# Kernel tuning notes

Measured on AMD Instinct MI355X. Metric: run time of the kernel, lower is better.

Reference implementation:

```python
import jax, jax.numpy as jnp
import numpy as np

B, S, H, D, P = 16, 512, 12, 768, 256
TOP_RATE = 0.1
K = int(round(TOP_RATE * S))  # 51, matches round(self.top_rate * hidden_state.size(1))
LN_EPS = 1e-5


def setup_inputs() -> dict:
    key = jax.random.key(0)
    ks = jax.random.split(key, 6)
    return {
        "hidden_state": jax.random.normal(ks[0], (B, S, D), dtype=jnp.float32),
        "attention": jax.random.normal(ks[1], (B, H, S, S), dtype=jnp.float32),
        "length": S,  # uniform valid length (scalar int)
        # node_trans: Linear(D, P)
        "W_node": jax.random.normal(ks[2], (D, P), dtype=jnp.float32) * 0.02,
        "b_node": jnp.zeros((P,), dtype=jnp.float32),
        # node_eta parameter, initialized to 0 (self.node_eta.data.fill_(0))
        "node_eta": jnp.zeros((1,), dtype=jnp.float32),
        # fc: Linear(P, P)
        "W_fc": jax.random.normal(ks[3], (P, P), dtype=jnp.float32) * 0.02,
        "b_fc": jnp.zeros((P,), dtype=jnp.float32),
        # LayerNorm(P)
        "ln_gamma": jnp.ones((P,), dtype=jnp.float32),
        "ln_beta": jnp.zeros((P,), dtype=jnp.float32),
    }


def reference(hidden_state, attention, W_node, b_node, node_eta, W_fc, b_fc,
              ln_gamma, ln_beta, length):
    # average attention over heads: [B, S, S]
    avg_atten = attention.mean(axis=1)
    # per-target-node top-k neighbors
    vals, idx = jax.lax.top_k(avg_atten, K)  # [B, S, K]
    # edge mask replicating softmax(where(v>0, v, -1e9)) followed by nonzero():
    # entries at -1e9 underflow to exactly 0 in fp32 softmax iff the row has a
    # positive value; otherwise the softmax is uniform and all edges survive.
    keep = vals > 0.0
    row_has_pos = keep.any(axis=-1, keepdims=True)
    keep = jnp.where(row_has_pos, keep, True)            # [B, S, K] (>=1 True per row)
    keepf = keep.astype(hidden_state.dtype)[..., None]   # [B, S, K, 1]

    # node_trans on all nodes: [B, S, P]
    h = hidden_state @ W_node + b_node

    # gather source-node features h[b, idx[b, t, j], :] -> [B, S, K, P]
    gathered = jax.vmap(lambda hb, ib: hb[ib])(h, idx)

    # reduce='mean': edge weight w=1, mailbox mean over kept incoming edges
    h_agg = (gathered * keepf).sum(axis=2) / keepf.sum(axis=2)

    eta = node_eta[0]
    new_h = eta * h + (1.0 - eta) * h_agg                # [B, S, P]

    # dgl.mean_nodes: mean over the `length` nodes of each sub-graph (=S here)
    out = new_h.mean(axis=1)                             # [B, P]

    # fc(dropout(tanh(out))) with dropout in eval mode (identity)
    out = jnp.tanh(out) @ W_fc + b_fc

    # LayerNorm
    mu = out.mean(axis=-1, keepdims=True)
    var = ((out - mu) ** 2).mean(axis=-1, keepdims=True)
    out = (out - mu) / jnp.sqrt(var + LN_EPS) * ln_gamma + ln_beta
    return out
```

## Files before the change

kernel.cpp:

```cpp
#include <hip/hip_runtime.h>
#include <math.h>

#define B_ 16
#define S_ 512
#define H_ 12
#define D_ 768
#define P_ 256
#define K_ 51
#define CH_ 16
#define NCHUNK_ (S_/CH_)

#define WAVE_SYNC() asm volatile("s_waitcnt lgkmcnt(0)" ::: "memory")

__device__ __forceinline__ unsigned okey(float f) {
  unsigned u = __float_as_uint(f);
  return (u & 0x80000000u) ? ~u : (u | 0x80000000u);
}

__global__ __launch_bounds__(256) void k1_topk_weights(
    const float* __restrict__ attn, float* __restrict__ w) {
  const int tid = threadIdx.x;
  const int wv = tid >> 6;
  const int lane = tid & 63;
  const int bt = blockIdx.x * 4 + wv;
  const int b = bt >> 9;
  const int t = bt & (S_ - 1);

  __shared__ __align__(16) unsigned hist[4][256];

  *(uint4*)&hist[wv][4 * lane] = uint4{0u, 0u, 0u, 0u};

  const float* base = attn + (((size_t)b * H_) * S_ + t) * S_;
  float a[8] = {0.f, 0.f, 0.f, 0.f, 0.f, 0.f, 0.f, 0.f};
  #pragma unroll
  for (int h = 0; h < H_; ++h) {
    const float* r = base + (size_t)h * (S_ * S_);
    const float4 u = *(const float4*)(r + 4 * lane);
    const float4 v = *(const float4*)(r + 256 + 4 * lane);
    a[0] += u.x; a[1] += u.y; a[2] += u.z; a[3] += u.w;
    a[4] += v.x; a[5] += v.y; a[6] += v.z; a[7] += v.w;
  }
  unsigned k[8];
  #pragma unroll
  for (int i = 0; i < 8; ++i) {
    a[i] *= (1.0f / (float)H_);
    k[i] = okey(a[i]);
  }

  int p = 0;
  #pragma unroll
  for (int i = 0; i < 8; ++i) p += __popcll(__ballot(a[i] > 0.f));

  bool sel[8];
  float invcnt;
  if (p >= 1 && p < K_) {
    #pragma unroll
    for (int i = 0; i < 8; ++i) sel[i] = (a[i] > 0.f);
    invcnt = 1.0f / (float)p;
  } else {
    unsigned prefix = 0;
    int remaining = K_;
    int tieCnt = 0;
    bool exited = false;
    unsigned exitm = 0;
    for (int pass = 0; pass < 4; ++pass) {
      const int shift = 24 - 8 * pass;
      const unsigned pm = (pass == 0) ? 0u : (0xFFFFFFFFu << (shift + 8));
      WAVE_SYNC();
      #pragma unroll
      for (int i = 0; i < 8; ++i)
        if ((k[i] & pm) == prefix)
          atomicAdd(&hist[wv][(k[i] >> shift) & 255u], 1u);
      WAVE_SYNC();
      const uint4 c4 = *(uint4*)&hist[wv][4 * lane];
      *(uint4*)&hist[wv][4 * lane] = uint4{0u, 0u, 0u, 0u};
      const unsigned loc = c4.x + c4.y + c4.z + c4.w;
      unsigned suf = loc;
      #pragma unroll
      for (int off = 1; off < 64; off <<= 1) {
        const unsigned vv = __shfl_down(suf, off, 64);
        if (lane + off < 64) suf += vv;
      }
      const unsigned after = suf - loc;
      const unsigned s3 = after + c4.w;
      const unsigned s2 = s3 + c4.z;
      const unsigned s1 = s2 + c4.y;
      const unsigned s0 = s1 + c4.x;
      const unsigned rem = (unsigned)remaining;
      int dig = 0, abv = 0, tie = 0;
      bool found = false;
      if (s0 >= rem && s1 < rem)         { dig = 4*lane+0; abv = (int)s1;    tie = (int)(s0 - s1);    found = true; }
      else if (s1 >= rem && s2 < rem)    { dig = 4*lane+1; abv = (int)s2;    tie = (int)(s1 - s2);    found = true; }
      else if (s2 >= rem && s3 < rem)    { dig = 4*lane+2; abv = (int)s3;    tie = (int)(s2 - s3);    found = true; }
      else if (s3 >= rem && after < rem) { dig = 4*lane+3; abv = (int)after; tie = (int)(s3 - after); found = true; }
      const unsigned long long fm = __ballot(found);
      const int src = __ffsll((unsigned long long)fm) - 1;
      dig = __shfl(dig, src, 64);
      abv = __shfl(abv, src, 64);
      tie = __shfl(tie, src, 64);
      prefix |= ((unsigned)dig) << shift;
      remaining -= abv;
      tieCnt = tie;
      if (tieCnt == remaining) {
        exited = true;
        exitm = (shift == 0) ? 0xFFFFFFFFu : (0xFFFFFFFFu << shift);
        break;
      }
    }
    if (exited) {
      #pragma unroll
      for (int i = 0; i < 8; ++i) sel[i] = (k[i] & exitm) >= prefix;
    } else {
      const unsigned T = prefix;
      unsigned long long m[8];
      #pragma unroll
      for (int i = 0; i < 8; ++i) m[i] = __ballot(k[i] == T);
      const unsigned long long lt = ((unsigned long long)1 << lane) - 1ull;
      int fh = 0;
      #pragma unroll
      for (int i = 0; i < 4; ++i) fh += __popcll(m[i]);
      #pragma unroll
      for (int i = 0; i < 8; ++i) {
        sel[i] = (k[i] > T);
        if (k[i] == T) {
          int r = 0;
          if (i < 4) {
            #pragma unroll
            for (int i2 = 0; i2 < 4; ++i2) r += __popcll(m[i2] & lt);
            for (int i2 = 0; i2 < i; ++i2) r += (int)((m[i2] >> lane) & 1ull);
          } else {
            r = fh;
            #pragma unroll
            for (int i2 = 4; i2 < 8; ++i2) r += __popcll(m[i2] & lt);
            for (int i2 = 4; i2 < i; ++i2) r += (int)((m[i2] >> lane) & 1ull);
          }
          if (r < remaining) sel[i] = true;
        }
      }
    }
    invcnt = 1.0f / (float)K_;
  }

  float* wrow = w + b * S_;
  #pragma unroll
  for (int i = 0; i < 8; ++i) {
    const int col = (i < 4) ? (4 * lane + i) : (256 + 4 * lane + (i - 4));
    if (sel[i]) atomicAdd(&wrow[col], invcnt);
  }
}

__global__ __launch_bounds__(192) void k2_weighted_sum(
    const float* __restrict__ hidden, const float* __restrict__ w,
    const float* __restrict__ node_eta, float* __restrict__ x) {
  const int chunk = blockIdx.x;
  const int b = blockIdx.y;
  const int tid = threadIdx.x;
  __shared__ float coef[CH_];
  if (tid < CH_) {
    const float eta = node_eta[0];
    const float wv = w[b * S_ + chunk * CH_ + tid];
    coef[tid] = (eta + (1.0f - eta) * wv) * (1.0f / (float)S_);
  }
  __syncthreads();
  const float* hb = hidden + ((size_t)b * S_ + (size_t)chunk * CH_) * D_ + 4 * tid;
  float4 acc = make_float4(0.f, 0.f, 0.f, 0.f);
  #pragma unroll
  for (int s = 0; s < CH_; ++s) {
    const float4 v = *(const float4*)(hb + (size_t)s * D_);
    const float c = coef[s];
    acc.x += c * v.x; acc.y += c * v.y; acc.z += c * v.z; acc.w += c * v.w;
  }
  float* xp = x + b * D_ + 4 * tid;
  atomicAdd(xp + 0, acc.x);
  atomicAdd(xp + 1, acc.y);
  atomicAdd(xp + 2, acc.z);
  atomicAdd(xp + 3, acc.w);
}

__global__ __launch_bounds__(256) void k3a_tanh_matvec(
    const float* __restrict__ x, const float* __restrict__ W_node,
    const float* __restrict__ b_node, float* __restrict__ tbuf) {
  const int j = blockIdx.x;
  const int b = blockIdx.y;
  const int tid = threadIdx.x;
  const int pp = tid & 15;
  const int g = tid >> 4;
  __shared__ float xs[D_];
  __shared__ float part[16][32];
  for (int d = tid; d < D_; d += 256) xs[d] = x[b * D_ + d];
  __syncthreads();
  const float* Wp = W_node + 32 * j + 2 * pp;
  float2 acc = make_float2(0.f, 0.f);
  const int d0 = 48 * g;
  #pragma unroll 8
  for (int dd = 0; dd < 48; ++dd) {
    const int d = d0 + dd;
    const float2 wv = *(const float2*)(Wp + (size_t)d * P_);
    const float xv = xs[d];
    acc.x += xv * wv.x; acc.y += xv * wv.y;
  }
  *(float2*)&part[g][2 * pp] = acc;
  __syncthreads();
  if (tid < 32) {
    float s = 0.f;
    #pragma unroll
    for (int gg = 0; gg < 16; ++gg) s += part[gg][tid];
    const int pcol = 32 * j + tid;
    tbuf[b * P_ + pcol] = tanhf(s + b_node[pcol]);
  }
}

__global__ __launch_bounds__(256) void k3b_fc(
    const float* __restrict__ tbuf, const float* __restrict__ W_fc,
    const float* __restrict__ b_fc, float* __restrict__ obuf) {
  const int j = blockIdx.x;
  const int b = blockIdx.y;
  const int tid = threadIdx.x;
  const int pp = tid & 31;
  const int g = tid >> 5;
  __shared__ float ts[P_];
  __shared__ float part[8][64];
  ts[tid] = tbuf[b * P_ + tid];
  __syncthreads();
  const float* Wp = W_fc + 64 * j + 2 * pp;
  float2 acc = make_float2(0.f, 0.f);
  const int q0 = 32 * g;
  #pragma unroll 8
  for (int qq = 0; qq < 32; ++qq) {
    const int q = q0 + qq;
    const float2 wv = *(const float2*)(Wp + (size_t)q * P_);
    const float tv = ts[q];
    acc.x += tv * wv.x; acc.y += tv * wv.y;
  }
  *(float2*)&part[g][2 * pp] = acc;
  __syncthreads();
  if (tid < 64) {
    float s = 0.f;
    #pragma unroll
    for (int gg = 0; gg < 8; ++gg) s += part[gg][tid];
    const int pcol = 64 * j + tid;
    obuf[b * P_ + pcol] = s + b_fc[pcol];
  }
}

__global__ __launch_bounds__(256) void k3c_layernorm(
    const float* __restrict__ obuf, const float* __restrict__ gamma,
    const float* __restrict__ beta, float* __restrict__ out) {
  const int b = blockIdx.x;
  const int tid = threadIdx.x;
  __shared__ float red[4];
  const float o = obuf[b * P_ + tid];
  float s = o;
  #pragma unroll
  for (int off = 32; off > 0; off >>= 1) s += __shfl_down(s, off, 64);
  const int wave = tid >> 6, lane = tid & 63;
  if (lane == 0) red[wave] = s;
  __syncthreads();
  const float mu = (red[0] + red[1] + red[2] + red[3]) * (1.0f / (float)P_);
  __syncthreads();
  const float dv = o - mu;
  float s2 = dv * dv;
  #pragma unroll
  for (int off = 32; off > 0; off >>= 1) s2 += __shfl_down(s2, off, 64);
  if (lane == 0) red[wave] = s2;
  __syncthreads();
  const float var = (red[0] + red[1] + red[2] + red[3]) * (1.0f / (float)P_);
  const float inv = 1.0f / sqrtf(var + 1e-5f);
  out[b * P_ + tid] = dv * inv * gamma[tid] + beta[tid];
}

extern "C" void kernel_launch(void* const* d_in, const int* in_sizes, int n_in,
                              void* d_out, int out_size, void* d_ws, size_t ws_size,
                              hipStream_t stream) {
  (void)in_sizes; (void)n_in; (void)out_size; (void)ws_size;
  const float* hidden   = (const float*)d_in[0];
  const float* attn     = (const float*)d_in[1];
  const float* W_node   = (const float*)d_in[3];
  const float* b_node   = (const float*)d_in[4];
  const float* node_eta = (const float*)d_in[5];
  const float* W_fc     = (const float*)d_in[6];
  const float* b_fc     = (const float*)d_in[7];
  const float* gamma    = (const float*)d_in[8];
  const float* beta     = (const float*)d_in[9];
  float* out = (float*)d_out;

  float* w    = (float*)d_ws;
  float* x    = w + B_ * S_;
  float* tbuf = x + B_ * D_;
  float* obuf = tbuf + B_ * P_;
  hipMemsetAsync(d_ws, 0, (size_t)(B_ * S_ + B_ * D_) * sizeof(float), stream);

  k1_topk_weights<<<(B_ * S_) / 4, 256, 0, stream>>>(attn, w);
  k2_weighted_sum<<<dim3(NCHUNK_, B_), 192, 0, stream>>>(hidden, w, node_eta, x);
  k3a_tanh_matvec<<<dim3(8, B_), 256, 0, stream>>>(x, W_node, b_node, tbuf);
  k3b_fc<<<dim3(4, B_), 256, 0, stream>>>(tbuf, W_fc, b_fc, obuf);
  k3c_layernorm<<<B_, 256, 0, stream>>>(obuf, gamma, beta, out);
}
```

Measured before the change: 340.7 us.

## Replace float atomics with bitmask ballots, bitwise radix select, fuse fc+layernorm

The top-k kernel now writes per-row selection bitmasks and an inverse count instead of doing global float atomicAdds into the column weight array. A new kernel sums those masks per column into the final coefficients. The radix select switches from an LDS histogram with atomics to a 32-pass bitwise select using ballot counts. The fc and layernorm kernels are merged into one launch, which removes one launch and the weight memset but adds a column-sum kernel that has low parallelism.

```diff
diff --git a/kernel.cpp b/kernel.cpp
--- a/kernel.cpp
+++ b/kernel.cpp
@@ -10,25 +10,20 @@
 #define CH_ 16
 #define NCHUNK_ (S_/CH_)
 
-#define WAVE_SYNC() asm volatile("s_waitcnt lgkmcnt(0)" ::: "memory")
-
 __device__ __forceinline__ unsigned okey(float f) {
   unsigned u = __float_as_uint(f);
   return (u & 0x80000000u) ? ~u : (u | 0x80000000u);
 }
 
-__global__ __launch_bounds__(256) void k1_topk_weights(
-    const float* __restrict__ attn, float* __restrict__ w) {
+__global__ __launch_bounds__(256) void k1_topk_mask(
+    const float* __restrict__ attn, unsigned long long* __restrict__ maskbuf,
+    float* __restrict__ invbuf) {
   const int tid = threadIdx.x;
   const int wv = tid >> 6;
   const int lane = tid & 63;
   const int bt = blockIdx.x * 4 + wv;
   const int b = bt >> 9;
   const int t = bt & (S_ - 1);
-
-  __shared__ __align__(16) unsigned hist[4][256];
-
-  *(uint4*)&hist[wv][4 * lane] = uint4{0u, 0u, 0u, 0u};
 
   const float* base = attn + (((size_t)b * H_) * S_ + t) * S_;
   float a[8] = {0.f, 0.f, 0.f, 0.f, 0.f, 0.f, 0.f, 0.f};
@@ -59,66 +54,33 @@
     invcnt = 1.0f / (float)p;
   } else {
     unsigned prefix = 0;
-    int remaining = K_;
-    int tieCnt = 0;
-    bool exited = false;
-    unsigned exitm = 0;
-    for (int pass = 0; pass < 4; ++pass) {
-      const int shift = 24 - 8 * pass;
-      const unsigned pm = (pass == 0) ? 0u : (0xFFFFFFFFu << (shift + 8));
-      WAVE_SYNC();
+    int rem = K_;
+    bool done = false;
+    unsigned dmask = 0, thr = 0;
+    for (int bpos = 31; bpos >= 0; --bpos) {
+      const unsigned bit = 1u << bpos;
+      const unsigned mb = ~(bit - 1u);
+      const unsigned cand = prefix | bit;
+      int cnt = 0;
       #pragma unroll
       for (int i = 0; i < 8; ++i)
-        if ((k[i] & pm) == prefix)
-          atomicAdd(&hist[wv][(k[i] >> shift) & 255u], 1u);
-      WAVE_SYNC();
-      const uint4 c4 = *(uint4*)&hist[wv][4 * lane];
-      *(uint4*)&hist[wv][4 * lane] = uint4{0u, 0u, 0u, 0u};
-      const unsigned loc = c4.x + c4.y + c4.z + c4.w;
-      unsigned suf = loc;
-      #pragma unroll
-      for (int off = 1; off < 64; off <<= 1) {
-        const unsigned vv = __shfl_down(suf, off, 64);
-        if (lane + off < 64) suf += vv;
-      }
-      const unsigned after = suf - loc;
-      const unsigned s3 = after + c4.w;
-      const unsigned s2 = s3 + c4.z;
-      const unsigned s1 = s2 + c4.y;
-      const unsigned s0 = s1 + c4.x;
-      const unsigned rem = (unsigned)remaining;
-      int dig = 0, abv = 0, tie = 0;
-      bool found = false;
-      if (s0 >= rem && s1 < rem)         { dig = 4*lane+0; abv = (int)s1;    tie = (int)(s0 - s1);    found = true; }
-      else if (s1 >= rem && s2 < rem)    { dig = 4*lane+1; abv = (int)s2;    tie = (int)(s1 - s2);    found = true; }
-      else if (s2 >= rem && s3 < rem)    { dig = 4*lane+2; abv = (int)s3;    tie = (int)(s2 - s3);    found = true; }
-      else if (s3 >= rem && after < rem) { dig = 4*lane+3; abv = (int)after; tie = (int)(s3 - after); found = true; }
-      const unsigned long long fm = __ballot(found);
-      const int src = __ffsll((unsigned long long)fm) - 1;
-      dig = __shfl(dig, src, 64);
-      abv = __shfl(abv, src, 64);
-      tie = __shfl(tie, src, 64);
-      prefix |= ((unsigned)dig) << shift;
-      remaining -= abv;
-      tieCnt = tie;
-      if (tieCnt == remaining) {
-        exited = true;
-        exitm = (shift == 0) ? 0xFFFFFFFFu : (0xFFFFFFFFu << shift);
-        break;
-      }
+        cnt += __popcll(__ballot((k[i] & mb) == cand));
+      if (cnt == rem) { done = true; dmask = mb; thr = cand; break; }
+      if (cnt > rem) prefix = cand;
+      else rem -= cnt;
     }
-    if (exited) {
-      #pragma unroll
-      for (int i = 0; i < 8; ++i) sel[i] = (k[i] & exitm) >= prefix;
+    if (done) {
+      #pragma unroll
+      for (int i = 0; i < 8; ++i) sel[i] = (k[i] & dmask) >= thr;
     } else {
       const unsigned T = prefix;
-      unsigned long long m[8];
-      #pragma unroll
-      for (int i = 0; i < 8; ++i) m[i] = __ballot(k[i] == T);
+      unsigned long long mm[8];
+      #pragma unroll
+      for (int i = 0; i < 8; ++i) mm[i] = __ballot(k[i] == T);
       const unsigned long long lt = ((unsigned long long)1 << lane) - 1ull;
       int fh = 0;
       #pragma unroll
-      for (int i = 0; i < 4; ++i) fh += __popcll(m[i]);
+      for (int i = 0; i < 4; ++i) fh += __popcll(mm[i]);
       #pragma unroll
       for (int i = 0; i < 8; ++i) {
         sel[i] = (k[i] > T);
@@ -126,48 +88,79 @@
           int r = 0;
           if (i < 4) {
             #pragma unroll
-            for (int i2 = 0; i2 < 4; ++i2) r += __popcll(m[i2] & lt);
-            for (int i2 = 0; i2 < i; ++i2) r += (int)((m[i2] >> lane) & 1ull);
+            for (int i2 = 0; i2 < 4; ++i2) r += __popcll(mm[i2] & lt);
+            for (int i2 = 0; i2 < i; ++i2) r += (int)((mm[i2] >> lane) & 1ull);
           } else {
             r = fh;
             #pragma unroll
-            for (int i2 = 4; i2 < 8; ++i2) r += __popcll(m[i2] & lt);
-            for (int i2 = 4; i2 < i; ++i2) r += (int)((m[i2] >> lane) & 1ull);
+            for (int i2 = 4; i2 < 8; ++i2) r += __popcll(mm[i2] & lt);
+            for (int i2 = 4; i2 < i; ++i2) r += (int)((mm[i2] >> lane) & 1ull);
           }
-          if (r < remaining) sel[i] = true;
+          if (r < rem) sel[i] = true;
         }
       }
     }
     invcnt = 1.0f / (float)K_;
   }
 
-  float* wrow = w + b * S_;
-  #pragma unroll
-  for (int i = 0; i < 8; ++i) {
-    const int col = (i < 4) ? (4 * lane + i) : (256 + 4 * lane + (i - 4));
-    if (sel[i]) atomicAdd(&wrow[col], invcnt);
-  }
+  unsigned long long m[8];
+  #pragma unroll
+  for (int i = 0; i < 8; ++i) m[i] = __ballot(sel[i]);
+  if (lane == 0) {
+    ulonglong2* mp = (ulonglong2*)(maskbuf + (size_t)bt * 8);
+    mp[0] = ulonglong2{m[0], m[1]};
+    mp[1] = ulonglong2{m[2], m[3]};
+    mp[2] = ulonglong2{m[4], m[5]};
+    mp[3] = ulonglong2{m[6], m[7]};
+    invbuf[bt] = invcnt;
+  }
+}
+
+__global__ __launch_bounds__(256) void k1b_colsum(
+    const unsigned long long* __restrict__ maskbuf,
+    const float* __restrict__ invbuf, const float* __restrict__ node_eta,
+    float* __restrict__ coef) {
+  const int half = blockIdx.x;
+  const int b = blockIdx.y;
+  const int tid = threadIdx.x;
+  __shared__ unsigned long long ms[S_][8];
+  __shared__ float inv[S_];
+
+  const ulonglong2* mrow2 = (const ulonglong2*)(maskbuf + (size_t)b * S_ * 8);
+  ulonglong2* lds2 = (ulonglong2*)&ms[0][0];
+  #pragma unroll
+  for (int j = 0; j < 8; ++j) lds2[tid + 256 * j] = mrow2[tid + 256 * j];
+  inv[tid] = invbuf[b * S_ + tid];
+  inv[tid + 256] = invbuf[b * S_ + tid + 256];
+  __syncthreads();
+
+  const int s = half * 256 + tid;
+  const int wi = (s < 256) ? (s & 3) : 4 + (s & 3);
+  const unsigned long long bitm = 1ull << ((s & 255) >> 2);
+  float w = 0.f;
+  #pragma unroll 8
+  for (int tt = 0; tt < S_; ++tt)
+    if (ms[tt][wi] & bitm) w += inv[tt];
+
+  const float eta = node_eta[0];
+  coef[b * S_ + s] = (eta + (1.0f - eta) * w) * (1.0f / (float)S_);
 }
 
 __global__ __launch_bounds__(192) void k2_weighted_sum(
-    const float* __restrict__ hidden, const float* __restrict__ w,
-    const float* __restrict__ node_eta, float* __restrict__ x) {
+    const float* __restrict__ hidden, const float* __restrict__ coef,
+    float* __restrict__ x) {
   const int chunk = blockIdx.x;
   const int b = blockIdx.y;
   const int tid = threadIdx.x;
-  __shared__ float coef[CH_];
-  if (tid < CH_) {
-    const float eta = node_eta[0];
-    const float wv = w[b * S_ + chunk * CH_ + tid];
-    coef[tid] = (eta + (1.0f - eta) * wv) * (1.0f / (float)S_);
-  }
+  __shared__ float cs[CH_];
+  if (tid < CH_) cs[tid] = coef[b * S_ + chunk * CH_ + tid];
   __syncthreads();
   const float* hb = hidden + ((size_t)b * S_ + (size_t)chunk * CH_) * D_ + 4 * tid;
   float4 acc = make_float4(0.f, 0.f, 0.f, 0.f);
   #pragma unroll
   for (int s = 0; s < CH_; ++s) {
     const float4 v = *(const float4*)(hb + (size_t)s * D_);
-    const float c = coef[s];
+    const float c = cs[s];
     acc.x += c * v.x; acc.y += c * v.y; acc.z += c * v.z; acc.w += c * v.w;
   }
   float* xp = x + b * D_ + 4 * tid;
@@ -210,46 +203,21 @@
   }
 }
 
-__global__ __launch_bounds__(256) void k3b_fc(
+__global__ __launch_bounds__(256) void k3bc_fc_ln(
     const float* __restrict__ tbuf, const float* __restrict__ W_fc,
-    const float* __restrict__ b_fc, float* __restrict__ obuf) {
-  const int j = blockIdx.x;
-  const int b = blockIdx.y;
-  const int tid = threadIdx.x;
-  const int pp = tid & 31;
-  const int g = tid >> 5;
-  __shared__ float ts[P_];
-  __shared__ float part[8][64];
-  ts[tid] = tbuf[b * P_ + tid];
-  __syncthreads();
-  const float* Wp = W_fc + 64 * j + 2 * pp;
-  float2 acc = make_float2(0.f, 0.f);
-  const int q0 = 32 * g;
-  #pragma unroll 8
-  for (int qq = 0; qq < 32; ++qq) {
-    const int q = q0 + qq;
-    const float2 wv = *(const float2*)(Wp + (size_t)q * P_);
-    const float tv = ts[q];
-    acc.x += tv * wv.x; acc.y += tv * wv.y;
-  }
-  *(float2*)&part[g][2 * pp] = acc;
-  __syncthreads();
-  if (tid < 64) {
-    float s = 0.f;
-    #pragma unroll
-    for (int gg = 0; gg < 8; ++gg) s += part[gg][tid];
-    const int pcol = 64 * j + tid;
-    obuf[b * P_ + pcol] = s + b_fc[pcol];
-  }
-}
-
-__global__ __launch_bounds__(256) void k3c_layernorm(
-    const float* __restrict__ obuf, const float* __restrict__ gamma,
+    const float* __restrict__ b_fc, const float* __restrict__ gamma,
     const float* __restrict__ beta, float* __restrict__ out) {
   const int b = blockIdx.x;
   const int tid = threadIdx.x;
+  __shared__ float ts[P_];
   __shared__ float red[4];
-  const float o = obuf[b * P_ + tid];
+  ts[tid] = tbuf[b * P_ + tid];
+  __syncthreads();
+  float acc = 0.f;
+  #pragma unroll 8
+  for (int q = 0; q < P_; ++q) acc += ts[q] * W_fc[(size_t)q * P_ + tid];
+  const float o = acc + b_fc[tid];
+
   float s = o;
   #pragma unroll
   for (int off = 32; off > 0; off >>= 1) s += __shfl_down(s, off, 64);
@@ -284,15 +252,17 @@
   const float* beta     = (const float*)d_in[9];
   float* out = (float*)d_out;
 
-  float* w    = (float*)d_ws;
-  float* x    = w + B_ * S_;
-  float* tbuf = x + B_ * D_;
-  float* obuf = tbuf + B_ * P_;
-  hipMemsetAsync(d_ws, 0, (size_t)(B_ * S_ + B_ * D_) * sizeof(float), stream);
-
-  k1_topk_weights<<<(B_ * S_) / 4, 256, 0, stream>>>(attn, w);
-  k2_weighted_sum<<<dim3(NCHUNK_, B_), 192, 0, stream>>>(hidden, w, node_eta, x);
+  unsigned long long* maskbuf = (unsigned long long*)d_ws;
+  float* invbuf = (float*)(maskbuf + (size_t)B_ * S_ * 8);
+  float* coef   = invbuf + B_ * S_;
+  float* x      = coef + B_ * S_;
+  float* tbuf   = x + B_ * D_;
+
+  hipMemsetAsync(x, 0, (size_t)(B_ * D_) * sizeof(float), stream);
+
+  k1_topk_mask<<<(B_ * S_) / 4, 256, 0, stream>>>(attn, maskbuf, invbuf);
+  k1b_colsum<<<dim3(2, B_), 256, 0, stream>>>(maskbuf, invbuf, node_eta, coef);
+  k2_weighted_sum<<<dim3(NCHUNK_, B_), 192, 0, stream>>>(hidden, coef, x);
   k3a_tanh_matvec<<<dim3(8, B_), 256, 0, stream>>>(x, W_node, b_node, tbuf);
-  k3b_fc<<<dim3(4, B_), 256, 0, stream>>>(tbuf, W_fc, b_fc, obuf);
-  k3c_layernorm<<<B_, 256, 0, stream>>>(obuf, gamma, beta, out);
-}
+  k3bc_fc_ln<<<B_, 256, 0, stream>>>(tbuf, W_fc, b_fc, gamma, beta, out);
+}
```

Measured after the change: 378.1 us. 1.11x slower.
